# Performance work log

Measured on AMD Instinct MI355X. Metric: run time of the kernel, lower is better.

Reference implementation:

```python
import jax, jax.numpy as jnp
import numpy as np

N_NODES = 100000
N_EDGES = 3200000
N_FEAT = 256
HIDDEN = 64
N_CLASSES = 6


def gcn_conv(x, W, b, src, dst, n_nodes):
    """PyG GCNConv: out = D^{-1/2} (A + I) D^{-1/2} X W + b (self-loops added)."""
    h = x @ W  # [N, out]
    loops = jnp.arange(n_nodes, dtype=src.dtype)
    src2 = jnp.concatenate([src, loops])
    dst2 = jnp.concatenate([dst, loops])
    # degree over destination nodes (edge weight 1), including self-loops
    deg = jax.ops.segment_sum(jnp.ones_like(dst2, dtype=h.dtype), dst2,
                              num_segments=n_nodes)
    dis = jnp.where(deg > 0, jax.lax.rsqrt(deg), 0.0)  # deg^{-1/2}
    norm = dis[src2] * dis[dst2]  # [E+N]
    msg = h[src2] * norm[:, None]  # gather + scale
    out = jax.ops.segment_sum(msg, dst2, num_segments=n_nodes)  # scatter-add
    return out + b


def setup_inputs() -> dict:
    key = jax.random.key(0)
    ks = jax.random.split(key, 5)
    x = jax.random.normal(ks[0], (N_NODES, N_FEAT), dtype=jnp.float32)
    edge_index = jax.random.randint(ks[1], (2, N_EDGES), 0, N_NODES, dtype=jnp.int64)
    W1 = jax.random.normal(ks[2], (N_FEAT, HIDDEN), dtype=jnp.float32) / np.sqrt(N_FEAT)
    b1 = jnp.zeros((HIDDEN,), dtype=jnp.float32)
    W2 = jax.random.normal(ks[3], (HIDDEN, HIDDEN), dtype=jnp.float32) / np.sqrt(HIDDEN)
    b2 = jnp.zeros((HIDDEN,), dtype=jnp.float32)
    Wfc = jax.random.normal(ks[4], (HIDDEN, N_CLASSES), dtype=jnp.float32) / np.sqrt(HIDDEN)
    bfc = jnp.zeros((N_CLASSES,), dtype=jnp.float32)
    return {"x": x, "edge_index": edge_index, "W1": W1, "b1": b1,
            "W2": W2, "b2": b2, "Wfc": Wfc, "bfc": bfc}


def reference(x, edge_index, W1, b1, W2, b2, Wfc, bfc):
    src, dst = edge_index[0], edge_index[1]
    n = x.shape[0]
    h = jax.nn.relu(gcn_conv(x, W1, b1, src, dst, n))
    # dropout(p=0.2) is identity in eval mode
    h = jax.nn.relu(gcn_conv(h, W2, b2, src, dst, n))
    return h @ Wfc + bfc
```

## Files before the change

kernel.cpp:

```cpp
#include <hip/hip_runtime.h>
#include <hip/hip_fp16.h>
#include <math.h>

#define NFEAT 256
#define HID 64
#define NCLS 6
#define NBMX 1600
#define CAPB 4096
#define CHUNK 8192
#define FUSED_LDS 45568

typedef float vf4 __attribute__((ext_vector_type(4)));
typedef int   vi4 __attribute__((ext_vector_type(4)));


__global__ __launch_bounds__(256) void k_count(const int* __restrict__ dst,
                                               int* __restrict__ C, int E, int nbuck) {
  __shared__ int cnt[NBMX];
  int t = threadIdx.x;
  for (int i = t; i < nbuck; i += 256) cnt[i] = 0;
  __syncthreads();
  int e0 = blockIdx.x * CHUNK;
  int e1 = e0 + CHUNK;
  if (e1 > E) e1 = E;
  for (int r0 = e0; r0 < e1; r0 += 1024) {
    int i0 = r0 + t * 4;
    if (i0 + 4 <= e1) {
      vi4 dv = __builtin_nontemporal_load((const vi4*)&dst[i0]);
      atomicAdd(&cnt[dv.x >> 6], 1);
      atomicAdd(&cnt[dv.y >> 6], 1);
      atomicAdd(&cnt[dv.z >> 6], 1);
      atomicAdd(&cnt[dv.w >> 6], 1);
    } else {
      for (int q = 0; q < 4; ++q)
        if (i0 + q < e1) atomicAdd(&cnt[dst[i0 + q] >> 6], 1);
    }
  }
  __syncthreads();
  int* Crow = C + (size_t)blockIdx.x * nbuck;
  for (int i = t; i < nbuck; i += 256) Crow[i] = cnt[i];
}


__global__ __launch_bounds__(256) void k_scan_cols(int* __restrict__ C,
                                                   int* __restrict__ T,
                                                   int nblk, int nbuck) {
  int b = blockIdx.x * 256 + threadIdx.x;
  if (b >= nbuck) return;
  int run = 0;
  int blk = 0;
  for (; blk + 4 <= nblk; blk += 4) {
    int c0 = C[(size_t)(blk + 0) * nbuck + b];
    int c1 = C[(size_t)(blk + 1) * nbuck + b];
    int c2 = C[(size_t)(blk + 2) * nbuck + b];
    int c3 = C[(size_t)(blk + 3) * nbuck + b];
    C[(size_t)(blk + 0) * nbuck + b] = run; run += c0;
    C[(size_t)(blk + 1) * nbuck + b] = run; run += c1;
    C[(size_t)(blk + 2) * nbuck + b] = run; run += c2;
    C[(size_t)(blk + 3) * nbuck + b] = run; run += c3;
  }
  for (; blk < nblk; ++blk) {
    int c = C[(size_t)blk * nbuck + b];
    C[(size_t)blk * nbuck + b] = run;
    run += c;
  }
  T[b] = run;
}


__global__ __launch_bounds__(256) void k_scanb(const int* __restrict__ T,
                                               int* __restrict__ bbase, int nbuck) {
  __shared__ int sh[256];
  __shared__ int carry;
  int t = threadIdx.x;
  if (t == 0) carry = 0;
  __syncthreads();
  for (int base = 0; base < nbuck; base += 256) {
    int v = (base + t < nbuck) ? T[base + t] : 0;
    sh[t] = v;
    __syncthreads();
    for (int off = 1; off < 256; off <<= 1) {
      int x = sh[t];
      int y = (t >= off) ? sh[t - off] : 0;
      __syncthreads();
      sh[t] = x + y;
      __syncthreads();
    }
    if (base + t < nbuck) bbase[base + t] = carry + sh[t] - v;
    __syncthreads();
    if (t == 255) carry += sh[255];
    __syncthreads();
  }
}


__global__ __launch_bounds__(256) void k_fused(const int* __restrict__ src,
                                               const int* __restrict__ dst,
                                               const int* __restrict__ C,
                                               const int* __restrict__ T,
                                               const int* __restrict__ bbase,
                                               unsigned* __restrict__ packed,
                                               int E, int nbuck, int nbb,
                                               const float* __restrict__ X,
                                               const float* __restrict__ W1,
                                               __half* __restrict__ H16, int n) {
  extern __shared__ char smem[];
  __shared__ int tsum[256];
  int t = threadIdx.x;

  if (blockIdx.x < nbb) {
    int* offs = (int*)smem;
    int* cur  = offs + NBMX;
    unsigned* entries = (unsigned*)(cur + NBMX);
    const int* Crow = C + (size_t)blockIdx.x * nbuck;
    bool last = (blockIdx.x == nbb - 1);
    const int* CrowN = C + (size_t)(blockIdx.x + 1) * nbuck;

    for (int b = t; b < nbuck; b += 256)
      offs[b] = (last ? T[b] : CrowN[b]) - Crow[b];
    __syncthreads();
    int base0 = t * 7;
    int c7[7];
    int s = 0;
#pragma unroll
    for (int i = 0; i < 7; ++i) {
      int b = base0 + i;
      c7[i] = (b < nbuck) ? offs[b] : 0;
      s += c7[i];
    }
    tsum[t] = s;
    __syncthreads();
    for (int off = 1; off < 256; off <<= 1) {
      int x = tsum[t];
      int y = (t >= off) ? tsum[t - off] : 0;
      __syncthreads();
      tsum[t] = x + y;
      __syncthreads();
    }
    int run = tsum[t] - s;
#pragma unroll
    for (int i = 0; i < 7; ++i) {
      int b = base0 + i;
      if (b < nbuck) { offs[b] = run; cur[b] = run; }
      run += c7[i];
    }
    __syncthreads();

    int e0 = blockIdx.x * CHUNK;
    int e1 = e0 + CHUNK;
    if (e1 > E) e1 = E;
    for (int r0 = e0; r0 < e1; r0 += 1024) {
      int i0 = r0 + t * 4;
      int s4[4], d4[4];
      bool full = (i0 + 4 <= e1);
      if (full) {
        vi4 sv = __builtin_nontemporal_load((const vi4*)&src[i0]);
        vi4 dv = __builtin_nontemporal_load((const vi4*)&dst[i0]);
        s4[0] = sv.x; s4[1] = sv.y; s4[2] = sv.z; s4[3] = sv.w;
        d4[0] = dv.x; d4[1] = dv.y; d4[2] = dv.z; d4[3] = dv.w;
      } else {
        for (int q = 0; q < 4; ++q)
          if (i0 + q < e1) { s4[q] = src[i0 + q]; d4[q] = dst[i0 + q]; }
      }
#pragma unroll
      for (int q = 0; q < 4; ++q) {
        if (i0 + q < e1) {
          int b = d4[q] >> 6;
          int p = atomicAdd(&cur[b], 1);
          entries[p] = ((unsigned)s4[q] << 6) | (unsigned)(d4[q] & 63);
        }
      }
    }
    __syncthreads();
    for (int b = t; b < nbuck; b += 256) {
      int lb = offs[b], le = cur[b];
      if (le > lb) {
        unsigned* g = &packed[(size_t)bbase[b] + Crow[b]];
        for (int k = lb; k < le; ++k) g[k - lb] = entries[k];
      }
    }
  } else {
    float* Wl = (float*)smem;
    float* Xl = Wl + 4096;
    const int row0 = (blockIdx.x - nbb) * 64;
    const int tc = t & 15;
    const int tr = t >> 4;
    float acc[4][4] = {};

    for (int k0 = 0; k0 < NFEAT; k0 += 64) {
      __syncthreads();
#pragma unroll
      for (int i = 0; i < 4; ++i) {
        int idx = t * 4 + i * 1024;
        int kr = idx >> 6, c = idx & 63;
        *(vf4*)&Wl[idx] = *(const vf4*)&W1[(size_t)(k0 + kr) * 64 + c];
      }
#pragma unroll
      for (int i = 0; i < 4; ++i) {
        int idx = t * 4 + i * 1024;
        int r = idx >> 6, c = idx & 63;
        int row = row0 + r;
        vf4 v = {0.f, 0.f, 0.f, 0.f};
        if (row < n) v = __builtin_nontemporal_load((const vf4*)&X[(size_t)row * NFEAT + k0 + c]);
        *(vf4*)&Xl[idx] = v;
      }
      __syncthreads();
#pragma unroll 4
      for (int kk = 0; kk < 64; kk += 4) {
        float4 xv[4], wv[4];
#pragma unroll
        for (int r = 0; r < 4; ++r) xv[r] = *(float4*)&Xl[(tr * 4 + r) * 64 + kk];
#pragma unroll
        for (int q = 0; q < 4; ++q) wv[q] = *(float4*)&Wl[(kk + q) * 64 + tc * 4];
#pragma unroll
        for (int r = 0; r < 4; ++r) {
          const float xr[4] = {xv[r].x, xv[r].y, xv[r].z, xv[r].w};
#pragma unroll
          for (int q = 0; q < 4; ++q) {
            acc[r][0] += xr[q] * wv[q].x;
            acc[r][1] += xr[q] * wv[q].y;
            acc[r][2] += xr[q] * wv[q].z;
            acc[r][3] += xr[q] * wv[q].w;
          }
        }
      }
    }
#pragma unroll
    for (int r = 0; r < 4; ++r) {
      int row = row0 + tr * 4 + r;
      if (row < n) {
        __half2 h01 = __floats2half2_rn(acc[r][0], acc[r][1]);
        __half2 h23 = __floats2half2_rn(acc[r][2], acc[r][3]);
        uint2 st;
        st.x = *reinterpret_cast<unsigned*>(&h01);
        st.y = *reinterpret_cast<unsigned*>(&h23);
        ((uint2*)H16)[(size_t)row * 16 + tc] = st;
      }
    }
  }
}


__global__ __launch_bounds__(256) void k_build(unsigned* __restrict__ packed,
                                               const int* __restrict__ T,
                                               const int* __restrict__ bbase,
                                               int2* __restrict__ rowrange,
                                               float* __restrict__ dis,
                                               int n, int nbuck) {
  __shared__ unsigned buf[CAPB];
  __shared__ unsigned outb[CAPB];
  __shared__ int cnt4[4][64];
  __shared__ int cur4[4][64];
  __shared__ int offi[64];
  __shared__ int offx[64];
  __shared__ int cntl[64];
  int b = blockIdx.x;
  int t = threadIdx.x;
  int g = t >> 6;
  int m = T[b];
  if (m > CAPB) m = CAPB;
  int bb = bbase[b];
  unsigned* pb = packed + bb;

  cnt4[g][t & 63] = 0;
  for (int k = t; k < m; k += 256) buf[k] = pb[k];
  __syncthreads();
  for (int k = t; k < m; k += 256) atomicAdd(&cnt4[g][buf[k] & 63u], 1);
  __syncthreads();
  if (t < 64) {
    int c0 = cnt4[0][t], c1 = cnt4[1][t], c2 = cnt4[2][t], c3 = cnt4[3][t];
    int tot = c0 + c1 + c2 + c3;
    cntl[t] = tot;
    offi[t] = tot;
    cur4[0][t] = 0;
    cur4[1][t] = c0;
    cur4[2][t] = c0 + c1;
    cur4[3][t] = c0 + c1 + c2;
  }
  __syncthreads();
  for (int off = 1; off < 64; off <<= 1) {
    int x = (t < 64) ? offi[t] : 0;
    int y = (t >= off && t < 64) ? offi[t - off] : 0;
    __syncthreads();
    if (t < 64) offi[t] = x + y;
    __syncthreads();
  }
  if (t < 64) {
    offx[t] = offi[t] - cntl[t];
    int v = b * 64 + t;
    if (v < n) {
      rowrange[v] = make_int2(bb + offx[t], cntl[t]);
      dis[v] = rsqrtf((float)cntl[t] + 1.0f);
    }
#pragma unroll
    for (int gg = 0; gg < 4; ++gg) cur4[gg][t] += offx[t];
  }
  __syncthreads();
  for (int k = t; k < m; k += 256) {
    unsigned e = buf[k];
    int dl = e & 63u;
    int q = atomicAdd(&cur4[g][dl], 1);
    outb[q] = e >> 6;
  }
  __syncthreads();
  for (int k = t; k < m; k += 256) pb[k] = outb[k];
}


__global__ __launch_bounds__(256) void k_agg_gemm(const int2* __restrict__ rowrange,
                                                  const int* __restrict__ srcs,
                                                  const __half* __restrict__ g16,
                                                  const float* __restrict__ dis,
                                                  const float* __restrict__ b1,
                                                  const float* __restrict__ W2,
                                                  __half* __restrict__ g2out, int n) {
  __shared__ float W2l[64 * 64];
  __shared__ float arow[16][68];
  int t = threadIdx.x;
  for (int i = t * 4; i < 4096; i += 1024)
    *(vf4*)&W2l[i] = *(const vf4*)&W2[i];

  int grp = t >> 4, lane = t & 15;
  int v = blockIdx.x * 16 + grp;
  bool active = (v < n);
  const uint2* g2 = (const uint2*)g16;

  float rx = 0.f, ry = 0.f, rz = 0.f, rw = 0.f;
  if (active) {
    int2 rr = rowrange[v];
    int j = rr.x, end = rr.x + rr.y;
    float dv = dis[v];
    uint2 su = g2[(size_t)v * 16 + lane];
    float2 f0 = __half22float2(*reinterpret_cast<__half2*>(&su.x));
    float2 f1 = __half22float2(*reinterpret_cast<__half2*>(&su.y));
    float ax = dv * f0.x, ay = dv * f0.y, az = dv * f1.x, aw = dv * f1.y;

    for (; j + 16 <= end; j += 16) {
      int s[16];
#pragma unroll
      for (int q = 0; q < 16; ++q) s[q] = __builtin_nontemporal_load(&srcs[j + q]);
      float ds[16];
      uint2 a[16];
#pragma unroll
      for (int q = 0; q < 16; ++q) { ds[q] = dis[s[q]]; a[q] = g2[(size_t)s[q] * 16 + lane]; }
#pragma unroll
      for (int q = 0; q < 16; ++q) {
        float2 p0 = __half22float2(*reinterpret_cast<__half2*>(&a[q].x));
        float2 p1 = __half22float2(*reinterpret_cast<__half2*>(&a[q].y));
        ax = fmaf(ds[q], p0.x, ax); ay = fmaf(ds[q], p0.y, ay);
        az = fmaf(ds[q], p1.x, az); aw = fmaf(ds[q], p1.y, aw);
      }
    }
    for (; j + 8 <= end; j += 8) {
      int s[8];
#pragma unroll
      for (int q = 0; q < 8; ++q) s[q] = __builtin_nontemporal_load(&srcs[j + q]);
      float ds[8];
      uint2 a[8];
#pragma unroll
      for (int q = 0; q < 8; ++q) { ds[q] = dis[s[q]]; a[q] = g2[(size_t)s[q] * 16 + lane]; }
#pragma unroll
      for (int q = 0; q < 8; ++q) {
        float2 p0 = __half22float2(*reinterpret_cast<__half2*>(&a[q].x));
        float2 p1 = __half22float2(*reinterpret_cast<__half2*>(&a[q].y));
        ax = fmaf(ds[q], p0.x, ax); ay = fmaf(ds[q], p0.y, ay);
        az = fmaf(ds[q], p1.x, az); aw = fmaf(ds[q], p1.y, aw);
      }
    }
    for (; j < end; ++j) {
      int s0 = __builtin_nontemporal_load(&srcs[j]);
      float ds = dis[s0];
      uint2 a0 = g2[(size_t)s0 * 16 + lane];
      float2 p0 = __half22float2(*reinterpret_cast<__half2*>(&a0.x));
      float2 p1 = __half22float2(*reinterpret_cast<__half2*>(&a0.y));
      ax = fmaf(ds, p0.x, ax); ay = fmaf(ds, p0.y, ay);
      az = fmaf(ds, p1.x, az); aw = fmaf(ds, p1.y, aw);
    }
    float4 bb = *(const float4*)&b1[lane * 4];
    rx = fmaxf(fmaf(dv, ax, bb.x), 0.f);
    ry = fmaxf(fmaf(dv, ay, bb.y), 0.f);
    rz = fmaxf(fmaf(dv, az, bb.z), 0.f);
    rw = fmaxf(fmaf(dv, aw, bb.w), 0.f);
  }
  arow[grp][lane * 4 + 0] = rx;
  arow[grp][lane * 4 + 1] = ry;
  arow[grp][lane * 4 + 2] = rz;
  arow[grp][lane * 4 + 3] = rw;
  __syncthreads();

  if (active) {
    float o0 = 0.f, o1 = 0.f, o2 = 0.f, o3 = 0.f;
    int c = lane * 4;
#pragma unroll 4
    for (int k = 0; k < 64; ++k) {
      float a = arow[grp][k];
      vf4 w = *(const vf4*)&W2l[k * 64 + c];
      o0 = fmaf(a, w.x, o0);
      o1 = fmaf(a, w.y, o1);
      o2 = fmaf(a, w.z, o2);
      o3 = fmaf(a, w.w, o3);
    }
    float dvv = dis[v];
    __half2 h01 = __floats2half2_rn(o0 * dvv, o1 * dvv);
    __half2 h23 = __floats2half2_rn(o2 * dvv, o3 * dvv);
    uint2 st;
    st.x = *reinterpret_cast<unsigned*>(&h01);
    st.y = *reinterpret_cast<unsigned*>(&h23);
    ((uint2*)g2out)[(size_t)v * 16 + lane] = st;
  }
}


__global__ __launch_bounds__(256) void k_agg_fc(const int2* __restrict__ rowrange,
                                                const int* __restrict__ srcs,
                                                const __half* __restrict__ g16,
                                                const float* __restrict__ dis,
                                                const float* __restrict__ b2,
                                                const float* __restrict__ Wfc,
                                                const float* __restrict__ bfc,
                                                float* __restrict__ outp, int n) {
  __shared__ float Wl[64 * NCLS];
  __shared__ float bl[8];
  int t = threadIdx.x;
  for (int i = t; i < 64 * NCLS; i += 256) Wl[i] = Wfc[i];
  if (t < NCLS) bl[t] = bfc[t];
  __syncthreads();

  int grp = t >> 4, lane = t & 15;
  int v = blockIdx.x * 16 + grp;
  bool active = (v < n);
  const uint2* g2 = (const uint2*)g16;

  float r0 = 0.f, r1 = 0.f, r2 = 0.f, r3 = 0.f;
  if (active) {
    int2 rr = rowrange[v];
    int j = rr.x, end = rr.x + rr.y;
    uint2 su = g2[(size_t)v * 16 + lane];
    float2 f0 = __half22float2(*reinterpret_cast<__half2*>(&su.x));
    float2 f1 = __half22float2(*reinterpret_cast<__half2*>(&su.y));
    float ax = f0.x, ay = f0.y, az = f1.x, aw = f1.y;

    for (; j + 16 <= end; j += 16) {
      int s[16];
#pragma unroll
      for (int q = 0; q < 16; ++q) s[q] = __builtin_nontemporal_load(&srcs[j + q]);
      uint2 a[16];
#pragma unroll
      for (int q = 0; q < 16; ++q) a[q] = g2[(size_t)s[q] * 16 + lane];
#pragma unroll
      for (int q = 0; q < 16; ++q) {
        float2 p0 = __half22float2(*reinterpret_cast<__half2*>(&a[q].x));
        float2 p1 = __half22float2(*reinterpret_cast<__half2*>(&a[q].y));
        ax += p0.x; ay += p0.y; az += p1.x; aw += p1.y;
      }
    }
    for (; j + 8 <= end; j += 8) {
      int s[8];
#pragma unroll
      for (int q = 0; q < 8; ++q) s[q] = __builtin_nontemporal_load(&srcs[j + q]);
      uint2 a[8];
#pragma unroll
      for (int q = 0; q < 8; ++q) a[q] = g2[(size_t)s[q] * 16 + lane];
#pragma unroll
      for (int q = 0; q < 8; ++q) {
        float2 p0 = __half22float2(*reinterpret_cast<__half2*>(&a[q].x));
        float2 p1 = __half22float2(*reinterpret_cast<__half2*>(&a[q].y));
        ax += p0.x; ay += p0.y; az += p1.x; aw += p1.y;
      }
    }
    for (; j < end; ++j) {
      int s0 = __builtin_nontemporal_load(&srcs[j]);
      uint2 a0 = g2[(size_t)s0 * 16 + lane];
      float2 p0 = __half22float2(*reinterpret_cast<__half2*>(&a0.x));
      float2 p1 = __half22float2(*reinterpret_cast<__half2*>(&a0.y));
      ax += p0.x; ay += p0.y; az += p1.x; aw += p1.y;
    }
    float dv = dis[v];
    float4 bb = *(const float4*)&b2[lane * 4];
    r0 = fmaxf(fmaf(dv, ax, bb.x), 0.f);
    r1 = fmaxf(fmaf(dv, ay, bb.y), 0.f);
    r2 = fmaxf(fmaf(dv, az, bb.z), 0.f);
    r3 = fmaxf(fmaf(dv, aw, bb.w), 0.f);
  }

  float p[NCLS];
#pragma unroll
  for (int jj = 0; jj < NCLS; ++jj) p[jj] = 0.f;
  int k0 = lane * 4;
#pragma unroll
  for (int q = 0; q < 4; ++q) {
    float a = (q == 0) ? r0 : (q == 1) ? r1 : (q == 2) ? r2 : r3;
#pragma unroll
    for (int jj = 0; jj < NCLS; ++jj)
      p[jj] = fmaf(a, Wl[(k0 + q) * NCLS + jj], p[jj]);
  }
#pragma unroll
  for (int m = 1; m < 16; m <<= 1) {
#pragma unroll
    for (int jj = 0; jj < NCLS; ++jj)
      p[jj] += __shfl_xor(p[jj], m, 64);
  }
  if (active && lane < NCLS)
    outp[(size_t)v * NCLS + lane] = p[lane] + bl[lane];
}


extern "C" void kernel_launch(void* const* d_in, const int* in_sizes, int n_in,
                              void* d_out, int out_size, void* d_ws, size_t ws_size,
                              hipStream_t stream) {
  const float* x   = (const float*)d_in[0];
  const int*   ei  = (const int*)d_in[1];
  const float* W1  = (const float*)d_in[2];
  const float* b1  = (const float*)d_in[3];
  const float* W2  = (const float*)d_in[4];
  const float* b2  = (const float*)d_in[5];
  const float* Wfc = (const float*)d_in[6];
  const float* bfc = (const float*)d_in[7];
  float* out = (float*)d_out;

  const int n = in_sizes[0] / NFEAT;
  const int E = in_sizes[1] / 2;
  const int* src = ei;
  const int* dst = ei + E;
  const int nbuck = (n + 63) >> 6;
  const int nbb = (E + CHUNK - 1) / CHUNK;
  const int ntile = (n + 63) / 64;

  char* ws = (char*)d_ws;
  size_t off = 0;
  auto alloc = [&](size_t bytes) -> void* {
    void* p = (void*)(ws + off);
    off += (bytes + 255) & ~(size_t)255;
    return p;
  };
  float* dis      = (float*)alloc((size_t)n * 4);
  int2*  rowrange = (int2*)alloc((size_t)n * 8);
  int*   C        = (int*)alloc((size_t)nbb * nbuck * 4);
  int*   T        = (int*)alloc((size_t)nbuck * 4);
  int*   bbase    = (int*)alloc((size_t)nbuck * 4);
  unsigned* packed = (unsigned*)alloc((size_t)E * 4);
  __half* bufA16  = (__half*)alloc((size_t)n * HID * 2);
  __half* bufC16  = (__half*)alloc((size_t)n * HID * 2);

  k_count<<<nbb, 256, 0, stream>>>(dst, C, E, nbuck);
  k_scan_cols<<<(nbuck + 255) / 256, 256, 0, stream>>>(C, T, nbb, nbuck);
  k_scanb<<<1, 256, 0, stream>>>(T, bbase, nbuck);
  k_fused<<<nbb + ntile, 256, FUSED_LDS, stream>>>(src, dst, C, T, bbase, packed,
                                                   E, nbuck, nbb, x, W1, bufA16, n);
  k_build<<<nbuck, 256, 0, stream>>>(packed, T, bbase, rowrange, dis, n, nbuck);

  k_agg_gemm<<<(n + 15) / 16, 256, 0, stream>>>(rowrange, (const int*)packed, bufA16,
                                                dis, b1, W2, bufC16, n);

  k_agg_fc<<<(n + 15) / 16, 256, 0, stream>>>(rowrange, (const int*)packed, bufC16,
                                              dis, b2, Wfc, bfc, out, n);
}
```

Baseline: 313.3 us.

## Split GEMM1 tiles between scatter and build kernels, drop 16-wide gather unroll

The first dense GEMM (X@W1) tiles are now split. The first TILES_A tiles still run alongside the edge scatter kernel, and the rest run as extra blocks in the bucket-build kernel, which now uses dynamic shared memory. The aim is to balance work across the two launches so the build phase no longer leaves compute units idle. The 16-edge unrolled gather loops in both aggregation kernels are also removed, which lowers register pressure in exchange for less memory-level parallelism per wave. The split point is a fixed constant tuned to this graph size.

After: 309.5 us. No clear change (-1.2%).

```diff
diff --git a/kernel.cpp b/kernel.cpp
--- a/kernel.cpp
+++ b/kernel.cpp
@@ -8,10 +8,76 @@
 #define NBMX 1600
 #define CAPB 4096
 #define CHUNK 8192
-#define FUSED_LDS 45568
+#define LDS_A 45568
+#define LDS_B 32768
+#define TILES_A 1100
 
 typedef float vf4 __attribute__((ext_vector_type(4)));
 typedef int   vi4 __attribute__((ext_vector_type(4)));
+
+
+__device__ __forceinline__ void gemm1_tile(char* smem, int tile, int t,
+                                           const float* __restrict__ X,
+                                           const float* __restrict__ W1,
+                                           __half* __restrict__ H16, int n) {
+  float* Wl = (float*)smem;
+  float* Xl = Wl + 4096;
+  const int row0 = tile * 64;
+  const int tc = t & 15;
+  const int tr = t >> 4;
+  float acc[4][4] = {};
+
+  for (int k0 = 0; k0 < NFEAT; k0 += 64) {
+    __syncthreads();
+#pragma unroll
+    for (int i = 0; i < 4; ++i) {
+      int idx = t * 4 + i * 1024;
+      int kr = idx >> 6, c = idx & 63;
+      *(vf4*)&Wl[idx] = *(const vf4*)&W1[(size_t)(k0 + kr) * 64 + c];
+    }
+#pragma unroll
+    for (int i = 0; i < 4; ++i) {
+      int idx = t * 4 + i * 1024;
+      int r = idx >> 6, c = idx & 63;
+      int row = row0 + r;
+      vf4 v = {0.f, 0.f, 0.f, 0.f};
+      if (row < n) v = __builtin_nontemporal_load((const vf4*)&X[(size_t)row * NFEAT + k0 + c]);
+      *(vf4*)&Xl[idx] = v;
+    }
+    __syncthreads();
+#pragma unroll 4
+    for (int kk = 0; kk < 64; kk += 4) {
+      float4 xv[4], wv[4];
+#pragma unroll
+      for (int r = 0; r < 4; ++r) xv[r] = *(float4*)&Xl[(tr * 4 + r) * 64 + kk];
+#pragma unroll
+      for (int q = 0; q < 4; ++q) wv[q] = *(float4*)&Wl[(kk + q) * 64 + tc * 4];
+#pragma unroll
+      for (int r = 0; r < 4; ++r) {
+        const float xr[4] = {xv[r].x, xv[r].y, xv[r].z, xv[r].w};
+#pragma unroll
+        for (int q = 0; q < 4; ++q) {
+          acc[r][0] += xr[q] * wv[q].x;
+          acc[r][1] += xr[q] * wv[q].y;
+          acc[r][2] += xr[q] * wv[q].z;
+          acc[r][3] += xr[q] * wv[q].w;
+        }
+      }
+    }
+  }
+#pragma unroll
+  for (int r = 0; r < 4; ++r) {
+    int row = row0 + tr * 4 + r;
+    if (row < n) {
+      __half2 h01 = __floats2half2_rn(acc[r][0], acc[r][1]);
+      __half2 h23 = __floats2half2_rn(acc[r][2], acc[r][3]);
+      uint2 st;
+      st.x = *reinterpret_cast<unsigned*>(&h01);
+      st.y = *reinterpret_cast<unsigned*>(&h23);
+      ((uint2*)H16)[(size_t)row * 16 + tc] = st;
+    }
+  }
+}
 
 
 __global__ __launch_bounds__(256) void k_count(const int* __restrict__ dst,
@@ -94,16 +160,16 @@
 }
 
 
-__global__ __launch_bounds__(256) void k_fused(const int* __restrict__ src,
-                                               const int* __restrict__ dst,
-                                               const int* __restrict__ C,
-                                               const int* __restrict__ T,
-                                               const int* __restrict__ bbase,
-                                               unsigned* __restrict__ packed,
-                                               int E, int nbuck, int nbb,
-                                               const float* __restrict__ X,
-                                               const float* __restrict__ W1,
-                                               __half* __restrict__ H16, int n) {
+__global__ __launch_bounds__(256) void k_fusedA(const int* __restrict__ src,
+                                                const int* __restrict__ dst,
+                                                const int* __restrict__ C,
+                                                const int* __restrict__ T,
+                                                const int* __restrict__ bbase,
+                                                unsigned* __restrict__ packed,
+                                                int E, int nbuck, int nbb,
+                                                const float* __restrict__ X,
+                                                const float* __restrict__ W1,
+                                                __half* __restrict__ H16, int n) {
   extern __shared__ char smem[];
   __shared__ int tsum[256];
   int t = threadIdx.x;
@@ -180,130 +246,83 @@
       }
     }
   } else {
-    float* Wl = (float*)smem;
-    float* Xl = Wl + 4096;
-    const int row0 = (blockIdx.x - nbb) * 64;
-    const int tc = t & 15;
-    const int tr = t >> 4;
-    float acc[4][4] = {};
-
-    for (int k0 = 0; k0 < NFEAT; k0 += 64) {
-      __syncthreads();
-#pragma unroll
-      for (int i = 0; i < 4; ++i) {
-        int idx = t * 4 + i * 1024;
-        int kr = idx >> 6, c = idx & 63;
-        *(vf4*)&Wl[idx] = *(const vf4*)&W1[(size_t)(k0 + kr) * 64 + c];
-      }
-#pragma unroll
-      for (int i = 0; i < 4; ++i) {
-        int idx = t * 4 + i * 1024;
-        int r = idx >> 6, c = idx & 63;
-        int row = row0 + r;
-        vf4 v = {0.f, 0.f, 0.f, 0.f};
-        if (row < n) v = __builtin_nontemporal_load((const vf4*)&X[(size_t)row * NFEAT + k0 + c]);
-        *(vf4*)&Xl[idx] = v;
-      }
-      __syncthreads();
-#pragma unroll 4
-      for (int kk = 0; kk < 64; kk += 4) {
-        float4 xv[4], wv[4];
-#pragma unroll
-        for (int r = 0; r < 4; ++r) xv[r] = *(float4*)&Xl[(tr * 4 + r) * 64 + kk];
-#pragma unroll
-        for (int q = 0; q < 4; ++q) wv[q] = *(float4*)&Wl[(kk + q) * 64 + tc * 4];
-#pragma unroll
-        for (int r = 0; r < 4; ++r) {
-          const float xr[4] = {xv[r].x, xv[r].y, xv[r].z, xv[r].w};
-#pragma unroll
-          for (int q = 0; q < 4; ++q) {
-            acc[r][0] += xr[q] * wv[q].x;
-            acc[r][1] += xr[q] * wv[q].y;
-            acc[r][2] += xr[q] * wv[q].z;
-            acc[r][3] += xr[q] * wv[q].w;
-          }
-        }
-      }
-    }
-#pragma unroll
-    for (int r = 0; r < 4; ++r) {
-      int row = row0 + tr * 4 + r;
-      if (row < n) {
-        __half2 h01 = __floats2half2_rn(acc[r][0], acc[r][1]);
-        __half2 h23 = __floats2half2_rn(acc[r][2], acc[r][3]);
-        uint2 st;
-        st.x = *reinterpret_cast<unsigned*>(&h01);
-        st.y = *reinterpret_cast<unsigned*>(&h23);
-        ((uint2*)H16)[(size_t)row * 16 + tc] = st;
-      }
-    }
-  }
-}
-
-
-__global__ __launch_bounds__(256) void k_build(unsigned* __restrict__ packed,
-                                               const int* __restrict__ T,
-                                               const int* __restrict__ bbase,
-                                               int2* __restrict__ rowrange,
-                                               float* __restrict__ dis,
-                                               int n, int nbuck) {
-  __shared__ unsigned buf[CAPB];
-  __shared__ unsigned outb[CAPB];
+    gemm1_tile(smem, blockIdx.x - nbb, t, X, W1, H16, n);
+  }
+}
+
+
+__global__ __launch_bounds__(256) void k_fusedB(unsigned* __restrict__ packed,
+                                                const int* __restrict__ T,
+                                                const int* __restrict__ bbase,
+                                                int2* __restrict__ rowrange,
+                                                float* __restrict__ dis,
+                                                int n, int nbuck,
+                                                const float* __restrict__ X,
+                                                const float* __restrict__ W1,
+                                                __half* __restrict__ H16, int tilesA) {
+  extern __shared__ char smem[];
   __shared__ int cnt4[4][64];
   __shared__ int cur4[4][64];
   __shared__ int offi[64];
   __shared__ int offx[64];
   __shared__ int cntl[64];
-  int b = blockIdx.x;
   int t = threadIdx.x;
-  int g = t >> 6;
-  int m = T[b];
-  if (m > CAPB) m = CAPB;
-  int bb = bbase[b];
-  unsigned* pb = packed + bb;
-
-  cnt4[g][t & 63] = 0;
-  for (int k = t; k < m; k += 256) buf[k] = pb[k];
-  __syncthreads();
-  for (int k = t; k < m; k += 256) atomicAdd(&cnt4[g][buf[k] & 63u], 1);
-  __syncthreads();
-  if (t < 64) {
-    int c0 = cnt4[0][t], c1 = cnt4[1][t], c2 = cnt4[2][t], c3 = cnt4[3][t];
-    int tot = c0 + c1 + c2 + c3;
-    cntl[t] = tot;
-    offi[t] = tot;
-    cur4[0][t] = 0;
-    cur4[1][t] = c0;
-    cur4[2][t] = c0 + c1;
-    cur4[3][t] = c0 + c1 + c2;
-  }
-  __syncthreads();
-  for (int off = 1; off < 64; off <<= 1) {
-    int x = (t < 64) ? offi[t] : 0;
-    int y = (t >= off && t < 64) ? offi[t - off] : 0;
-    __syncthreads();
-    if (t < 64) offi[t] = x + y;
-    __syncthreads();
-  }
-  if (t < 64) {
-    offx[t] = offi[t] - cntl[t];
-    int v = b * 64 + t;
-    if (v < n) {
-      rowrange[v] = make_int2(bb + offx[t], cntl[t]);
-      dis[v] = rsqrtf((float)cntl[t] + 1.0f);
-    }
-#pragma unroll
-    for (int gg = 0; gg < 4; ++gg) cur4[gg][t] += offx[t];
-  }
-  __syncthreads();
-  for (int k = t; k < m; k += 256) {
-    unsigned e = buf[k];
-    int dl = e & 63u;
-    int q = atomicAdd(&cur4[g][dl], 1);
-    outb[q] = e >> 6;
-  }
-  __syncthreads();
-  for (int k = t; k < m; k += 256) pb[k] = outb[k];
+
+  if (blockIdx.x < (unsigned)nbuck) {
+    unsigned* buf  = (unsigned*)smem;
+    unsigned* outb = buf + CAPB;
+    int b = blockIdx.x;
+    int g = t >> 6;
+    int m = T[b];
+    if (m > CAPB) m = CAPB;
+    int bb = bbase[b];
+    unsigned* pb = packed + bb;
+
+    cnt4[g][t & 63] = 0;
+    for (int k = t; k < m; k += 256) buf[k] = pb[k];
+    __syncthreads();
+    for (int k = t; k < m; k += 256) atomicAdd(&cnt4[g][buf[k] & 63u], 1);
+    __syncthreads();
+    if (t < 64) {
+      int c0 = cnt4[0][t], c1 = cnt4[1][t], c2 = cnt4[2][t], c3 = cnt4[3][t];
+      int tot = c0 + c1 + c2 + c3;
+      cntl[t] = tot;
+      offi[t] = tot;
+      cur4[0][t] = 0;
+      cur4[1][t] = c0;
+      cur4[2][t] = c0 + c1;
+      cur4[3][t] = c0 + c1 + c2;
+    }
+    __syncthreads();
+    for (int off = 1; off < 64; off <<= 1) {
+      int x = (t < 64) ? offi[t] : 0;
+      int y = (t >= off && t < 64) ? offi[t - off] : 0;
+      __syncthreads();
+      if (t < 64) offi[t] = x + y;
+      __syncthreads();
+    }
+    if (t < 64) {
+      offx[t] = offi[t] - cntl[t];
+      int v = b * 64 + t;
+      if (v < n) {
+        rowrange[v] = make_int2(bb + offx[t], cntl[t]);
+        dis[v] = rsqrtf((float)cntl[t] + 1.0f);
+      }
+#pragma unroll
+      for (int gg = 0; gg < 4; ++gg) cur4[gg][t] += offx[t];
+    }
+    __syncthreads();
+    for (int k = t; k < m; k += 256) {
+      unsigned e = buf[k];
+      int dl = e & 63u;
+      int q = atomicAdd(&cur4[g][dl], 1);
+      outb[q] = e >> 6;
+    }
+    __syncthreads();
+    for (int k = t; k < m; k += 256) pb[k] = outb[k];
+  } else {
+    gemm1_tile(smem, tilesA + (int)blockIdx.x - nbuck, t, X, W1, H16, n);
+  }
 }
 
 
@@ -335,22 +354,6 @@
     float2 f1 = __half22float2(*reinterpret_cast<__half2*>(&su.y));
     float ax = dv * f0.x, ay = dv * f0.y, az = dv * f1.x, aw = dv * f1.y;
 
-    for (; j + 16 <= end; j += 16) {
-      int s[16];
-#pragma unroll
-      for (int q = 0; q < 16; ++q) s[q] = __builtin_nontemporal_load(&srcs[j + q]);
-      float ds[16];
-      uint2 a[16];
-#pragma unroll
-      for (int q = 0; q < 16; ++q) { ds[q] = dis[s[q]]; a[q] = g2[(size_t)s[q] * 16 + lane]; }
-#pragma unroll
-      for (int q = 0; q < 16; ++q) {
-        float2 p0 = __half22float2(*reinterpret_cast<__half2*>(&a[q].x));
-        float2 p1 = __half22float2(*reinterpret_cast<__half2*>(&a[q].y));
-        ax = fmaf(ds[q], p0.x, ax); ay = fmaf(ds[q], p0.y, ay);
-        az = fmaf(ds[q], p1.x, az); aw = fmaf(ds[q], p1.y, aw);
-      }
-    }
     for (; j + 8 <= end; j += 8) {
       int s[8];
 #pragma unroll
@@ -440,20 +443,6 @@
     float2 f1 = __half22float2(*reinterpret_cast<__half2*>(&su.y));
     float ax = f0.x, ay = f0.y, az = f1.x, aw = f1.y;
 
-    for (; j + 16 <= end; j += 16) {
-      int s[16];
-#pragma unroll
-      for (int q = 0; q < 16; ++q) s[q] = __builtin_nontemporal_load(&srcs[j + q]);
-      uint2 a[16];
-#pragma unroll
-      for (int q = 0; q < 16; ++q) a[q] = g2[(size_t)s[q] * 16 + lane];
-#pragma unroll
-      for (int q = 0; q < 16; ++q) {
-        float2 p0 = __half22float2(*reinterpret_cast<__half2*>(&a[q].x));
-        float2 p1 = __half22float2(*reinterpret_cast<__half2*>(&a[q].y));
-        ax += p0.x; ay += p0.y; az += p1.x; aw += p1.y;
-      }
-    }
     for (; j + 8 <= end; j += 8) {
       int s[8];
 #pragma unroll
@@ -525,6 +514,9 @@
   const int nbuck = (n + 63) >> 6;
   const int nbb = (E + CHUNK - 1) / CHUNK;
   const int ntile = (n + 63) / 64;
+  int tilesA = TILES_A;
+  if (tilesA > ntile) tilesA = ntile;
+  const int tilesB = ntile - tilesA;
 
   char* ws = (char*)d_ws;
   size_t off = 0;
@@ -545,9 +537,10 @@
   k_count<<<nbb, 256, 0, stream>>>(dst, C, E, nbuck);
   k_scan_cols<<<(nbuck + 255) / 256, 256, 0, stream>>>(C, T, nbb, nbuck);
   k_scanb<<<1, 256, 0, stream>>>(T, bbase, nbuck);
-  k_fused<<<nbb + ntile, 256, FUSED_LDS, stream>>>(src, dst, C, T, bbase, packed,
-                                                   E, nbuck, nbb, x, W1, bufA16, n);
-  k_build<<<nbuck, 256, 0, stream>>>(packed, T, bbase, rowrange, dis, n, nbuck);
+  k_fusedA<<<nbb + tilesA, 256, LDS_A, stream>>>(src, dst, C, T, bbase, packed,
+                                                 E, nbuck, nbb, x, W1, bufA16, n);
+  k_fusedB<<<nbuck + tilesB, 256, LDS_B, stream>>>(packed, T, bbase, rowrange, dis,
+                                                   n, nbuck, x, W1, bufA16, tilesA);
 
   k_agg_gemm<<<(n + 15) / 16, 256, 0, stream>>>(rowrange, (const int*)packed, bufA16,
                                                 dis, b1, W2, bufC16, n);
```
